# Performance work log

Hardware: AMD Instinct MI355X
Metric: run time of the kernel (lower is better)

## Reference

```python
import jax, jax.numpy as jnp
import numpy as np

B, T, D = 4, 4096, 1024

def setup_inputs() -> dict:
    key = jax.random.key(0)
    ks = jax.random.split(key, 7)
    s1 = 1.0 / np.sqrt(D)
    s2 = 1.0 / np.sqrt(2 * D)
    return {
        "x": jax.random.normal(ks[0], (B, T, D), jnp.float32),
        "W1": jax.random.uniform(ks[1], (D, 2 * D), jnp.float32, -s1, s1),      # Linear(D,2D,bias=False)
        "W2": jax.random.uniform(ks[2], (2 * D, 2 * D), jnp.float32, -s2, s2),  # Linear(2D,2D)
        "b2": jax.random.uniform(ks[3], (2 * D,), jnp.float32, -s2, s2),
        "conv_w": jax.random.uniform(ks[4], (D, 1, 3), jnp.float32, -1/np.sqrt(3), 1/np.sqrt(3)),  # depthwise k=3
        "gamma": jnp.ones((D,), jnp.float32),
        "beta": jnp.zeros((D,), jnp.float32),
    }

def _gated_scan(theta, alpha):
    # parallel stable scan: h_t = a_t * h_{t-1} + (1 - a_t) * tanh(theta_t), h_0 = 0
    a = jax.nn.sigmoid(alpha)
    b = (1.0 - a) * jnp.tanh(theta)
    def combine(c1, c2):
        a1, b1 = c1
        a2, b2 = c2
        return a1 * a2, a2 * b1 + b2
    _, h = jax.lax.associative_scan(combine, (a, b), axis=1)
    return h

def reference(x, W1, W2, b2, conv_w, gamma, beta):
    # morphism generator: Linear -> SiLU -> Linear
    mp = jax.nn.silu(x @ W1) @ W2 + b2                      # (B,T,2D)
    theta, alpha = jnp.split(mp, 2, axis=-1)
    semantic = _gated_scan(theta, alpha)                    # (B,T,D)
    # causal depthwise conv: left-pad 2, kernel 3, groups=D
    sc = jnp.transpose(semantic, (0, 2, 1))                 # (B,D,T)
    cb = jax.lax.conv_general_dilated(
        sc, conv_w, window_strides=(1,), padding=[(2, 0)],
        dimension_numbers=("NCH", "OIH", "NCH"), feature_group_count=D)
    cb = jax.nn.silu(jnp.transpose(cb, (0, 2, 1)))          # (B,T,D)
    y = semantic + 0.1 * cb
    # LayerNorm over D
    mu = jnp.mean(y, axis=-1, keepdims=True)
    var = jnp.mean(jnp.square(y - mu), axis=-1, keepdims=True)
    y = (y - mu) * jax.lax.rsqrt(var + 1e-5) * gamma + beta
    # dropout is identity in eval mode; L2 normalize (torch eps=1e-12)
    nrm = jnp.sqrt(jnp.sum(jnp.square(y), axis=-1, keepdims=True))
    return y / jnp.maximum(nrm, 1e-12)
```

## Files before the change

kernel.cpp:

```cpp
#include <hip/hip_runtime.h>
#include <cstdint>
#include <cstddef>

typedef __attribute__((ext_vector_type(8))) short bf16x8;
typedef __attribute__((ext_vector_type(4))) float f32x4;
typedef unsigned short u16;
typedef unsigned int u32;

__device__ __forceinline__ u16 f2bf(float f) {
  u32 u = __float_as_uint(f);
  u32 r = (u + 0x7fffu + ((u >> 16) & 1u)) >> 16;
  return (u16)r;
}
__device__ __forceinline__ float bf2f(u16 h) {
  return __uint_as_float(((u32)h) << 16);
}
__device__ __forceinline__ float fsilu(float v) { return v / (1.f + __expf(-v)); }
__device__ __forceinline__ float fsigmoid(float v) { return 1.f / (1.f + __expf(-v)); }

__device__ __forceinline__ void glds16(const void* g, void* l) {
  __builtin_amdgcn_global_load_lds(
      (const __attribute__((address_space(1))) void*)g,
      (__attribute__((address_space(3))) void*)l, 16, 0, 0);
}

#define FENCE_MEM() asm volatile("" ::: "memory")
#define BAR() __builtin_amdgcn_s_barrier()
#define VMCNT(n) asm volatile("s_waitcnt vmcnt(" #n ")" ::: "memory")
#define LGKM0() asm volatile("s_waitcnt lgkmcnt(0)" ::: "memory")
#define SFENCE() __builtin_amdgcn_sched_barrier(0)


__global__ __launch_bounds__(256) void cast_bf16_vec(const float* __restrict__ src,
                                                     u16* __restrict__ dst, int n4) {
  int i = blockIdx.x * 256 + threadIdx.x;
  if (i >= n4) return;
  const float4 v = ((const float4*)src)[i];
  ushort4 o;
  o.x = f2bf(v.x); o.y = f2bf(v.y); o.z = f2bf(v.z); o.w = f2bf(v.w);
  ((ushort4*)dst)[i] = o;
}

__global__ void transpose_cast(const float* __restrict__ src, u16* __restrict__ dst,
                               int R, int C) {
  __shared__ float tile[32][33];
  int bx = blockIdx.x * 32;
  int by = blockIdx.y * 32;
  int tx = threadIdx.x, ty = threadIdx.y;
#pragma unroll
  for (int i = 0; i < 4; ++i)
    tile[ty + i * 8][tx] = src[(size_t)(by + ty + i * 8) * C + bx + tx];
  __syncthreads();
#pragma unroll
  for (int i = 0; i < 4; ++i)
    dst[(size_t)(bx + ty + i * 8) * R + by + tx] = f2bf(tile[tx][ty + i * 8]);
}


template <int EPI>
__global__ __launch_bounds__(512, 2) void gemm256(const u16* __restrict__ A,
                                                  const u16* __restrict__ Bt,
                                                  u16* __restrict__ Co,
                                                  const float* __restrict__ bias,
                                                  int M, int N, int K) {
  __shared__ char lds[131072];
  const int tid = threadIdx.x;
  const int lane = tid & 63;
  const int wid = tid >> 6;
  const int wr = wid >> 2;
  const int wc = wid & 3;

  const int gx = gridDim.x;
  const int nwg = gx * gridDim.y;
  const int bid = blockIdx.y * gx + blockIdx.x;
  const int swz = (bid & 7) * (nwg >> 3) + (bid >> 3);
  const long bm = (long)(swz / gx) * 256;
  const long bn = (long)(swz % gx) * 256;

  const int NT = K >> 6;

  const int r0 = tid >> 3, c0p = tid & 7;
  const int r1 = r0 + 64;
  const int gA0 = (r0 & 63) + ((r0 >> 6) << 7);
  const int gA1 = (r1 & 63) + ((r1 >> 6) << 7);
  const int gB0 = (r0 & 31) + ((r0 >> 5) << 6);
  const int gB1 = (r1 & 31) + ((r1 >> 5) << 6);
  const int cA0 = c0p ^ (r0 & 7);
  const size_t srcA0 = (size_t)(bm + gA0) * K + cA0 * 8;
  const size_t srcA1 = (size_t)(bm + gA1) * K + cA0 * 8;
  const size_t srcB0 = (size_t)(bn + gB0) * K + cA0 * 8;
  const size_t srcB1 = (size_t)(bn + gB1) * K + cA0 * 8;
  const int dstA0 = gA0 * 128 + c0p * 16;
  const int dstA1 = gA1 * 128 + c0p * 16;
  const int dstB0 = 32768 + gB0 * 128 + c0p * 16;
  const int dstB1 = 32768 + gB1 * 128 + c0p * 16;
  const size_t halfA = (size_t)64 * K;
  const size_t halfB = (size_t)32 * K;

#define STAGE_A(buf, half, t)                                                        \
  do {                                                                               \
    glds16(A + srcA0 + (half) * halfA + (size_t)(t) * 64,                            \
           lds + (buf) * 65536 + dstA0 + (half) * 8192);                             \
    glds16(A + srcA1 + (half) * halfA + (size_t)(t) * 64,                            \
           lds + (buf) * 65536 + dstA1 + (half) * 8192);                             \
  } while (0)
#define STAGE_B(buf, half, t)                                                        \
  do {                                                                               \
    glds16(Bt + srcB0 + (half) * halfB + (size_t)(t) * 64,                           \
           lds + (buf) * 65536 + dstB0 + (half) * 4096);                             \
    glds16(Bt + srcB1 + (half) * halfB + (size_t)(t) * 64,                           \
           lds + (buf) * 65536 + dstB1 + (half) * 4096);                             \
  } while (0)

  const int l15 = lane & 15, l3 = lane & 7, g4 = lane >> 4;
  const int aoff0 = (wr * 128 + l15) * 128 + ((g4 ^ l3) * 16);
  const int aoff1 = (wr * 128 + l15) * 128 + (((4 + g4) ^ l3) * 16);
  const int boff0 = 32768 + (wc * 64 + l15) * 128 + ((g4 ^ l3) * 16);
  const int boff1 = 32768 + (wc * 64 + l15) * 128 + (((4 + g4) ^ l3) * 16);

  f32x4 acc[8][4] = {};

#define PHASEQ(q, STMT, TAIL)                                                        \
  do {                                                                               \
    bf16x8 af[2][2];                                                                 \
    _Pragma("unroll") for (int mm = 0; mm < 2; ++mm) {                               \
      af[mm][0] = *(const bf16x8*)(base + aoff0 + ((q) * 2 + mm) * 2048);            \
      af[mm][1] = *(const bf16x8*)(base + aoff1 + ((q) * 2 + mm) * 2048);            \
    }                                                                                \
    STMT;                                                                            \
    FENCE_MEM();                                                                     \
    BAR();                                                                           \
    LGKM0();                                                                         \
    SFENCE();                                                                        \
    __builtin_amdgcn_s_setprio(1);                                                   \
    _Pragma("unroll") for (int mm = 0; mm < 2; ++mm)                                 \
        _Pragma("unroll") for (int nn = 0; nn < 4; ++nn) {                           \
      acc[(q) * 2 + mm][nn] = __builtin_amdgcn_mfma_f32_16x16x32_bf16(               \
          af[mm][0], bfr[nn][0], acc[(q) * 2 + mm][nn], 0, 0, 0);                    \
      acc[(q) * 2 + mm][nn] = __builtin_amdgcn_mfma_f32_16x16x32_bf16(               \
          af[mm][1], bfr[nn][1], acc[(q) * 2 + mm][nn], 0, 0, 0);                    \
    }                                                                                \
    __builtin_amdgcn_s_setprio(0);                                                   \
    TAIL;                                                                            \
    BAR();                                                                           \
    FENCE_MEM();                                                                     \
  } while (0)

  STAGE_A(0, 0, 0);
  STAGE_A(0, 1, 0);
  STAGE_B(0, 0, 0);
  STAGE_B(0, 1, 0);
  FENCE_MEM();
  if (NT > 1) {
    STAGE_A(1, 0, 1);
    STAGE_B(1, 0, 1);
  }
  VMCNT(4);
  BAR();
  FENCE_MEM();

  for (int t = 0; t < NT; ++t) {
    const int p = t & 1;
    const char* base = lds + p * 65536;
    const bool s1 = (t + 1) < NT;
    const bool s2 = (t + 2) < NT;
    bf16x8 bfr[4][2];

    {
      bf16x8 af[2][2];
#pragma unroll
      for (int nn = 0; nn < 4; ++nn) {
        bfr[nn][0] = *(const bf16x8*)(base + boff0 + nn * 2048);
        bfr[nn][1] = *(const bf16x8*)(base + boff1 + nn * 2048);
      }
#pragma unroll
      for (int mm = 0; mm < 2; ++mm) {
        af[mm][0] = *(const bf16x8*)(base + aoff0 + mm * 2048);
        af[mm][1] = *(const bf16x8*)(base + aoff1 + mm * 2048);
      }
      if (s1) STAGE_A(p ^ 1, 1, t + 1);
      FENCE_MEM();
      BAR();
      LGKM0();
      SFENCE();
      __builtin_amdgcn_s_setprio(1);
#pragma unroll
      for (int mm = 0; mm < 2; ++mm)
#pragma unroll
        for (int nn = 0; nn < 4; ++nn) {
          acc[mm][nn] = __builtin_amdgcn_mfma_f32_16x16x32_bf16(
              af[mm][0], bfr[nn][0], acc[mm][nn], 0, 0, 0);
          acc[mm][nn] = __builtin_amdgcn_mfma_f32_16x16x32_bf16(
              af[mm][1], bfr[nn][1], acc[mm][nn], 0, 0, 0);
        }
      __builtin_amdgcn_s_setprio(0);
      BAR();
      FENCE_MEM();
    }
    PHASEQ(1, { if (s1) STAGE_B(p ^ 1, 1, t + 1); }, {});
    PHASEQ(2, { if (s2) STAGE_A(p, 0, t + 2); }, {});
    PHASEQ(3, { if (s2) STAGE_B(p, 0, t + 2); },
           { if (s2) { VMCNT(4); } else { VMCNT(0); } });
  }

  const int erow = (lane >> 4) * 4;
  const int ecol = lane & 15;
#pragma unroll
  for (int mf = 0; mf < 8; ++mf) {
#pragma unroll
    for (int nf = 0; nf < 4; ++nf) {
      const long col = bn + wc * 64 + nf * 16 + ecol;
      float badd = (EPI == 1) ? bias[col] : 0.f;
#pragma unroll
      for (int j = 0; j < 4; ++j) {
        const long row = bm + wr * 128 + mf * 16 + erow + j;
        float v = acc[mf][nf][j];
        if (EPI == 0) {
          v = fsilu(v);
        } else {
          v += badd;
          v = (col < 1024) ? tanhf(v) : fsigmoid(v);
        }
        Co[row * (long)N + col] = f2bf(v);
      }
    }
  }
#undef STAGE_A
#undef STAGE_B
#undef PHASEQ
}


__global__ __launch_bounds__(256) void scan_stage1(const u16* __restrict__ sa,
                                                   float* __restrict__ cA,
                                                   float* __restrict__ cB) {
  const int tid = blockIdx.x * 256 + threadIdx.x;
  const int d = tid & 1023;
  const int chunk = (tid >> 10) & 63;
  const int b = tid >> 16;
  const size_t base = ((size_t)(b * 4096 + chunk * 64)) * 2048 + d;
  float Ac = 1.f, Bc = 0.f;
#pragma unroll 4
  for (int t = 0; t < 64; ++t) {
    float s = bf2f(sa[base + (size_t)t * 2048]);
    float a = bf2f(sa[base + (size_t)t * 2048 + 1024]);
    Bc = a * Bc + (1.f - a) * s;
    Ac *= a;
  }
  cA[tid] = Ac;
  cB[tid] = Bc;
}

__global__ __launch_bounds__(256) void scan_stage2(const float* __restrict__ cA,
                                                   const float* __restrict__ cB,
                                                   float* __restrict__ hstart) {
  const int tid = blockIdx.x * 256 + threadIdx.x;
  const int d = tid & 1023;
  const int b = tid >> 10;
  float h = 0.f;
  for (int c = 0; c < 64; ++c) {
    const size_t i = ((size_t)(b * 64 + c)) * 1024 + d;
    hstart[i] = h;
    h = cA[i] * h + cB[i];
  }
}

__global__ __launch_bounds__(256) void scan_stage3(const u16* __restrict__ sa,
                                                   const float* __restrict__ hstart,
                                                   float* __restrict__ sem) {
  const int tid = blockIdx.x * 256 + threadIdx.x;
  const int d = tid & 1023;
  const int chunk = (tid >> 10) & 63;
  const int b = tid >> 16;
  const size_t m0 = (size_t)(b * 4096 + chunk * 64);
  const size_t base = m0 * 2048 + d;
  float h = hstart[tid];
#pragma unroll 4
  for (int t = 0; t < 64; ++t) {
    float s = bf2f(sa[base + (size_t)t * 2048]);
    float a = bf2f(sa[base + (size_t)t * 2048 + 1024]);
    h = a * h + (1.f - a) * s;
    sem[(m0 + t) * 1024 + d] = h;
  }
}


__global__ __launch_bounds__(256) void finalize(const float* __restrict__ sem,
                                                const float* __restrict__ cw,
                                                const float* __restrict__ gamma,
                                                const float* __restrict__ beta,
                                                float* __restrict__ out) {
  const int r = blockIdx.x;
  const int t = r & 4095;
  const int tid = threadIdx.x;
  const int lane = tid & 63, wid = tid >> 6;
  const int d0 = tid * 4;
  const float4 zero = make_float4(0.f, 0.f, 0.f, 0.f);
  float4 s0 = ((const float4*)(sem + (size_t)r * 1024))[tid];
  float4 s1 = (t >= 1) ? ((const float4*)(sem + (size_t)(r - 1) * 1024))[tid] : zero;
  float4 s2 = (t >= 2) ? ((const float4*)(sem + (size_t)(r - 2) * 1024))[tid] : zero;
  float a0[4] = {s0.x, s0.y, s0.z, s0.w};
  float a1[4] = {s1.x, s1.y, s1.z, s1.w};
  float a2[4] = {s2.x, s2.y, s2.z, s2.w};
  float y[4];
  float vs = 0.f, vq = 0.f;
#pragma unroll
  for (int j = 0; j < 4; ++j) {
    int d = d0 + j;
    float cb = cw[d * 3] * a2[j] + cw[d * 3 + 1] * a1[j] + cw[d * 3 + 2] * a0[j];
    cb = fsilu(cb);
    y[j] = a0[j] + 0.1f * cb;
    vs += y[j];
    vq += y[j] * y[j];
  }
  __shared__ float rb[2][4];
#pragma unroll
  for (int o = 32; o > 0; o >>= 1) {
    vs += __shfl_down(vs, o);
    vq += __shfl_down(vq, o);
  }
  if (lane == 0) { rb[0][wid] = vs; rb[1][wid] = vq; }
  __syncthreads();
  float tsum = rb[0][0] + rb[0][1] + rb[0][2] + rb[0][3];
  float tss = rb[1][0] + rb[1][1] + rb[1][2] + rb[1][3];
  float mu = tsum * (1.f / 1024.f);
  float var = tss * (1.f / 1024.f) - mu * mu;
  float rstd = rsqrtf(var + 1e-5f);
  float yn[4];
  float q = 0.f;
#pragma unroll
  for (int j = 0; j < 4; ++j) {
    int d = d0 + j;
    yn[j] = (y[j] - mu) * rstd * gamma[d] + beta[d];
    q += yn[j] * yn[j];
  }
#pragma unroll
  for (int o = 32; o > 0; o >>= 1) q += __shfl_down(q, o);
  __syncthreads();
  if (lane == 0) rb[0][wid] = q;
  __syncthreads();
  float nrm = sqrtf(rb[0][0] + rb[0][1] + rb[0][2] + rb[0][3]);
  float scale = 1.f / fmaxf(nrm, 1e-12f);
  float4 o4 = make_float4(yn[0] * scale, yn[1] * scale, yn[2] * scale, yn[3] * scale);
  ((float4*)(out + (size_t)r * 1024))[tid] = o4;
}


extern "C" void kernel_launch(void* const* d_in, const int* in_sizes, int n_in,
                              void* d_out, int out_size, void* d_ws, size_t ws_size,
                              hipStream_t stream) {
  const float* x = (const float*)d_in[0];
  const float* W1 = (const float*)d_in[1];
  const float* W2 = (const float*)d_in[2];
  const float* b2 = (const float*)d_in[3];
  const float* cw = (const float*)d_in[4];
  const float* gamma = (const float*)d_in[5];
  const float* beta = (const float*)d_in[6];
  float* out = (float*)d_out;
  char* ws = (char*)d_ws;

  u16* xb = (u16*)(ws);
  u16* w1t = (u16*)(ws + 33554432);
  u16* w2t = (u16*)(ws + 37748736);
  u16* h1 = (u16*)(ws + 46137344);
  float* sem = (float*)(ws + 46137344);
  u16* sa = (u16*)(ws + 113246208);
  float* cA = (float*)(ws);
  float* cB = (float*)(ws + 1048576);
  float* hstart = (float*)(ws + 2097152);

  cast_bf16_vec<<<16384, 256, 0, stream>>>(x, xb, 4194304);
  transpose_cast<<<dim3(64, 32), dim3(32, 8), 0, stream>>>(W1, w1t, 1024, 2048);
  transpose_cast<<<dim3(64, 64), dim3(32, 8), 0, stream>>>(W2, w2t, 2048, 2048);
  gemm256<0><<<dim3(8, 64), 512, 0, stream>>>(xb, w1t, h1, nullptr, 16384, 2048, 1024);
  gemm256<1><<<dim3(8, 64), 512, 0, stream>>>(h1, w2t, sa, b2, 16384, 2048, 2048);
  scan_stage1<<<1024, 256, 0, stream>>>(sa, cA, cB);
  scan_stage2<<<16, 256, 0, stream>>>(cA, cB, hstart);
  scan_stage3<<<1024, 256, 0, stream>>>(sa, hstart, sem);
  finalize<<<16384, 256, 0, stream>>>(sem, cw, gamma, beta, out);
}
```

Before: 344.4 us.

## Replace four-phase split prefetch GEMM pipeline with simple whole-tile double buffering

Replaces the four-phase GEMM main loop with a plain double-buffered loop. The old loop interleaved half-tile A/B global-to-LDS loads with barriers between MFMA groups and kept loads two tiles ahead. The new loop issues the whole next tile up front, runs all four MFMA quarters without barriers, then waits for all loads and syncs once per tile. This cuts barrier and waitcnt overhead, but prefetch depth drops to one tile and the fine-grained overlap of loads with compute is lost.

```diff
diff --git a/kernel.cpp b/kernel.cpp
--- a/kernel.cpp
+++ b/kernel.cpp
@@ -27,8 +27,6 @@
 #define FENCE_MEM() asm volatile("" ::: "memory")
 #define BAR() __builtin_amdgcn_s_barrier()
 #define VMCNT(n) asm volatile("s_waitcnt vmcnt(" #n ")" ::: "memory")
-#define LGKM0() asm volatile("s_waitcnt lgkmcnt(0)" ::: "memory")
-#define SFENCE() __builtin_amdgcn_sched_barrier(0)
 
 
 __global__ __launch_bounds__(256) void cast_bf16_vec(const float* __restrict__ src,
@@ -97,19 +95,20 @@
   const size_t halfA = (size_t)64 * K;
   const size_t halfB = (size_t)32 * K;
 
-#define STAGE_A(buf, half, t)                                                        \
+#define STAGE_ALL(buf, t)                                                            \
   do {                                                                               \
-    glds16(A + srcA0 + (half) * halfA + (size_t)(t) * 64,                            \
-           lds + (buf) * 65536 + dstA0 + (half) * 8192);                             \
-    glds16(A + srcA1 + (half) * halfA + (size_t)(t) * 64,                            \
-           lds + (buf) * 65536 + dstA1 + (half) * 8192);                             \
-  } while (0)
-#define STAGE_B(buf, half, t)                                                        \
-  do {                                                                               \
-    glds16(Bt + srcB0 + (half) * halfB + (size_t)(t) * 64,                           \
-           lds + (buf) * 65536 + dstB0 + (half) * 4096);                             \
-    glds16(Bt + srcB1 + (half) * halfB + (size_t)(t) * 64,                           \
-           lds + (buf) * 65536 + dstB1 + (half) * 4096);                             \
+    glds16(A + srcA0 + (size_t)(t) * 64, lds + (buf) * 65536 + dstA0);               \
+    glds16(A + srcA1 + (size_t)(t) * 64, lds + (buf) * 65536 + dstA1);               \
+    glds16(A + srcA0 + halfA + (size_t)(t) * 64,                                     \
+           lds + (buf) * 65536 + dstA0 + 8192);                                      \
+    glds16(A + srcA1 + halfA + (size_t)(t) * 64,                                     \
+           lds + (buf) * 65536 + dstA1 + 8192);                                      \
+    glds16(Bt + srcB0 + (size_t)(t) * 64, lds + (buf) * 65536 + dstB0);              \
+    glds16(Bt + srcB1 + (size_t)(t) * 64, lds + (buf) * 65536 + dstB1);              \
+    glds16(Bt + srcB0 + halfB + (size_t)(t) * 64,                                    \
+           lds + (buf) * 65536 + dstB0 + 4096);                                      \
+    glds16(Bt + srcB1 + halfB + (size_t)(t) * 64,                                    \
+           lds + (buf) * 65536 + dstB1 + 4096);                                      \
   } while (0)
 
   const int l15 = lane & 15, l3 = lane & 7, g4 = lane >> 4;
@@ -120,87 +119,50 @@
 
   f32x4 acc[8][4] = {};
 
-#define PHASEQ(q, STMT, TAIL)                                                        \
-  do {                                                                               \
-    bf16x8 af[2][2];                                                                 \
-    _Pragma("unroll") for (int mm = 0; mm < 2; ++mm) {                               \
-      af[mm][0] = *(const bf16x8*)(base + aoff0 + ((q) * 2 + mm) * 2048);            \
-      af[mm][1] = *(const bf16x8*)(base + aoff1 + ((q) * 2 + mm) * 2048);            \
-    }                                                                                \
-    STMT;                                                                            \
-    FENCE_MEM();                                                                     \
-    BAR();                                                                           \
-    LGKM0();                                                                         \
-    SFENCE();                                                                        \
-    __builtin_amdgcn_s_setprio(1);                                                   \
-    _Pragma("unroll") for (int mm = 0; mm < 2; ++mm)                                 \
-        _Pragma("unroll") for (int nn = 0; nn < 4; ++nn) {                           \
-      acc[(q) * 2 + mm][nn] = __builtin_amdgcn_mfma_f32_16x16x32_bf16(               \
-          af[mm][0], bfr[nn][0], acc[(q) * 2 + mm][nn], 0, 0, 0);                    \
-      acc[(q) * 2 + mm][nn] = __builtin_amdgcn_mfma_f32_16x16x32_bf16(               \
-          af[mm][1], bfr[nn][1], acc[(q) * 2 + mm][nn], 0, 0, 0);                    \
-    }                                                                                \
-    __builtin_amdgcn_s_setprio(0);                                                   \
-    TAIL;                                                                            \
-    BAR();                                                                           \
-    FENCE_MEM();                                                                     \
-  } while (0)
-
-  STAGE_A(0, 0, 0);
-  STAGE_A(0, 1, 0);
-  STAGE_B(0, 0, 0);
-  STAGE_B(0, 1, 0);
+  STAGE_ALL(0, 0);
+  VMCNT(0);
   FENCE_MEM();
-  if (NT > 1) {
-    STAGE_A(1, 0, 1);
-    STAGE_B(1, 0, 1);
-  }
-  VMCNT(4);
   BAR();
   FENCE_MEM();
 
   for (int t = 0; t < NT; ++t) {
     const int p = t & 1;
     const char* base = lds + p * 65536;
-    const bool s1 = (t + 1) < NT;
-    const bool s2 = (t + 2) < NT;
+
+    if (t + 1 < NT) STAGE_ALL(p ^ 1, t + 1);
+    FENCE_MEM();
+
     bf16x8 bfr[4][2];
-
-    {
+#pragma unroll
+    for (int nn = 0; nn < 4; ++nn) {
+      bfr[nn][0] = *(const bf16x8*)(base + boff0 + nn * 2048);
+      bfr[nn][1] = *(const bf16x8*)(base + boff1 + nn * 2048);
+    }
+#pragma unroll
+    for (int q = 0; q < 4; ++q) {
       bf16x8 af[2][2];
 #pragma unroll
-      for (int nn = 0; nn < 4; ++nn) {
-        bfr[nn][0] = *(const bf16x8*)(base + boff0 + nn * 2048);
-        bfr[nn][1] = *(const bf16x8*)(base + boff1 + nn * 2048);
+      for (int mm = 0; mm < 2; ++mm) {
+        af[mm][0] = *(const bf16x8*)(base + aoff0 + (q * 2 + mm) * 2048);
+        af[mm][1] = *(const bf16x8*)(base + aoff1 + (q * 2 + mm) * 2048);
       }
-#pragma unroll
-      for (int mm = 0; mm < 2; ++mm) {
-        af[mm][0] = *(const bf16x8*)(base + aoff0 + mm * 2048);
-        af[mm][1] = *(const bf16x8*)(base + aoff1 + mm * 2048);
-      }
-      if (s1) STAGE_A(p ^ 1, 1, t + 1);
-      FENCE_MEM();
-      BAR();
-      LGKM0();
-      SFENCE();
       __builtin_amdgcn_s_setprio(1);
 #pragma unroll
       for (int mm = 0; mm < 2; ++mm)
 #pragma unroll
         for (int nn = 0; nn < 4; ++nn) {
-          acc[mm][nn] = __builtin_amdgcn_mfma_f32_16x16x32_bf16(
-              af[mm][0], bfr[nn][0], acc[mm][nn], 0, 0, 0);
-          acc[mm][nn] = __builtin_amdgcn_mfma_f32_16x16x32_bf16(
-              af[mm][1], bfr[nn][1], acc[mm][nn], 0, 0, 0);
+          acc[q * 2 + mm][nn] = __builtin_amdgcn_mfma_f32_16x16x32_bf16(
+              af[mm][0], bfr[nn][0], acc[q * 2 + mm][nn], 0, 0, 0);
+          acc[q * 2 + mm][nn] = __builtin_amdgcn_mfma_f32_16x16x32_bf16(
+              af[mm][1], bfr[nn][1], acc[q * 2 + mm][nn], 0, 0, 0);
         }
       __builtin_amdgcn_s_setprio(0);
-      BAR();
-      FENCE_MEM();
     }
-    PHASEQ(1, { if (s1) STAGE_B(p ^ 1, 1, t + 1); }, {});
-    PHASEQ(2, { if (s2) STAGE_A(p, 0, t + 2); }, {});
-    PHASEQ(3, { if (s2) STAGE_B(p, 0, t + 2); },
-           { if (s2) { VMCNT(4); } else { VMCNT(0); } });
+
+    VMCNT(0);
+    FENCE_MEM();
+    BAR();
+    FENCE_MEM();
   }
 
   const int erow = (lane >> 4) * 4;
@@ -225,9 +187,7 @@
       }
     }
   }
-#undef STAGE_A
-#undef STAGE_B
-#undef PHASEQ
+#undef STAGE_ALL
 }
 
 
```

Result: no change. 340.6 us (-1.1%).
